# Kernel tuning notes

Measured on AMD Instinct MI355X. Metric: run time of the kernel, lower is better.

The kernel has to match this reference:

```python
import jax, jax.numpy as jnp
import numpy as np

N, R, E, DIN, DOUT, B = 40000, 16, 50000, 256, 256, 4


def setup_inputs() -> dict:
    key = jax.random.key(0)
    ks = jax.random.split(key, 7)
    xav = (2.0 / (DIN + DOUT)) ** 0.5  # xavier-ish scale
    x = jax.random.normal(ks[0], (N, DIN), jnp.float32)
    bases = jax.random.normal(ks[1], (B, DIN, DOUT), jnp.float32) * xav
    coeff = jax.random.normal(ks[2], (R, B), jnp.float32) * 0.5
    loop_weight = jax.random.normal(ks[3], (DIN, DOUT), jnp.float32) * xav
    h_bias = jnp.zeros((DOUT,), jnp.float32)
    edge_src = jax.random.randint(ks[4], (R, E), 0, N, dtype=jnp.int64)
    edge_dst = jax.random.randint(ks[5], (R, E), 0, N, dtype=jnp.int64)
    return {"x": x, "bases": bases, "coeff": coeff, "loop_weight": loop_weight,
            "h_bias": h_bias, "edge_src": edge_src, "edge_dst": edge_dst}


def reference(x, bases, coeff, loop_weight, h_bias, edge_src, edge_dst):
    # Basis decomposition: per-relation weight W_r = sum_b coeff[r,b] * bases[b]
    W = jnp.einsum('rb,bio->rio', coeff, bases)  # [R, DIN, DOUT]
    n = x.shape[0]

    def body(acc, rel):
        W_r, src, dst = rel
        # transform all nodes once, gather at edge sources
        m = (x @ W_r)[src]                                   # [E, DOUT]
        agg = jax.ops.segment_sum(m, dst, num_segments=n)    # [N, DOUT]
        deg = jax.ops.segment_sum(jnp.ones(src.shape, jnp.float32), dst,
                                  num_segments=n)            # in-degree per rel
        # norm='right': divide by dst in-degree (clamped to 1)
        return acc + agg / jnp.clip(deg, 1.0)[:, None], None

    h0 = jnp.zeros((n, loop_weight.shape[1]), x.dtype)
    h, _ = jax.lax.scan(body, h0, (W, edge_src, edge_dst))   # sum over relations
    h = h + x @ loop_weight + h_bias                         # self-loop + bias
    return jax.nn.relu(h)
```

## Files before the change

kernel.cpp:

```cpp
#include <hip/hip_runtime.h>

#define NN   40000
#define RR   16
#define EE   50000
#define DD   256
#define NB   4
#define KTOT (NB*DD + DD)
#define BM   64
#define BN   128
#define BK   32
#define NITER (KTOT/BK)

#define SCAN_BLK  40
#define SCAN_ELEM 1024

typedef __bf16 bf16x8 __attribute__((ext_vector_type(8)));
typedef float  f32x4  __attribute__((ext_vector_type(4)));
typedef float  f32x2  __attribute__((ext_vector_type(2)));
typedef unsigned short ushort_t;

__device__ inline unsigned short f2bf(float f) {
    unsigned int b = __builtin_bit_cast(unsigned int, f);
    b += 0x7FFFu + ((b >> 16) & 1u);
    return (unsigned short)(b >> 16);
}


#define CAST_BLKS ((NN * DD / 4 + DD * KTOT + 255) / 256)
#define DEG_BLKS  ((RR * EE + 255) / 256)

__global__ __launch_bounds__(256) void k_prep(const float* __restrict__ x,
                                              const float* __restrict__ bases,
                                              const float* __restrict__ lw,
                                              const int* __restrict__ edst,
                                              ushort_t* __restrict__ xb,
                                              ushort_t* __restrict__ Bt,
                                              int* __restrict__ deg) {
    int b = blockIdx.x;
    if (b < CAST_BLKS) {
        int t = b * 256 + threadIdx.x;
        const int NX = NN * DD / 4;
        if (t < NX) {
            float4 f = *(const float4*)(x + (size_t)t * 4);
            ushort4 o;
            o.x = f2bf(f.x); o.y = f2bf(f.y); o.z = f2bf(f.z); o.w = f2bf(f.w);
            *(ushort4*)(xb + (size_t)t * 4) = o;
        } else {
            int u = t - NX;
            if (u < DD * KTOT) {
                int o = u / KTOT, k = u - o * KTOT;
                float f = (k < NB * DD) ? bases[(size_t)k * DD + o]
                                        : lw[(size_t)(k - NB * DD) * DD + o];
                Bt[u] = f2bf(f);
            }
        }
    } else {
        int e = (b - CAST_BLKS) * 256 + threadIdx.x;
        if (e < RR * EE) {
            int r = e / EE;
            atomicAdd(&deg[r * NN + edst[e]], 1);
        }
    }
}

__global__ __launch_bounds__(256) void k_scanA(const int* __restrict__ deg,
                                               int* __restrict__ offsets,
                                               int* __restrict__ bsum) {
    __shared__ int part[256];
    int t = threadIdx.x, b = blockIdx.x;
    int g = b * SCAN_ELEM + t * 4;
    int4 h = {0, 0, 0, 0};
    if (g < NN) {
#pragma unroll
        for (int r = 0; r < RR; r++) {
            int4 d = *(const int4*)(deg + (size_t)r * NN + g);
            h.x += d.x; h.y += d.y; h.z += d.z; h.w += d.w;
        }
    }
    int s = h.x + h.y + h.z + h.w;
    part[t] = s;
    __syncthreads();
    for (int off = 1; off < 256; off <<= 1) {
        int v = (t >= off) ? part[t - off] : 0;
        __syncthreads();
        part[t] += v;
        __syncthreads();
    }
    int ex = part[t] - s;
    if (g < NN) {
        int4 o;
        o.x = ex;
        o.y = ex + h.x;
        o.z = ex + h.x + h.y;
        o.w = ex + h.x + h.y + h.z;
        *(int4*)(offsets + g) = o;
    }
    if (t == 255) bsum[b] = part[255];
}

__global__ __launch_bounds__(256) void k_scanB(const int* __restrict__ bsum,
                                               int* __restrict__ offsets,
                                               int* __restrict__ cursor) {
    __shared__ int sbase, stot;
    int t = threadIdx.x, b = blockIdx.x;
    if (t == 0) {
        int acc = 0, base = 0;
        for (int i = 0; i < SCAN_BLK; i++) {
            if (i == b) base = acc;
            acc += bsum[i];
        }
        sbase = base;
        stot = acc;
    }
    __syncthreads();
    int base = sbase;
    int g = b * SCAN_ELEM + t * 4;
    if (g < NN) {
        int4 o = *(const int4*)(offsets + g);
        o.x += base; o.y += base; o.z += base; o.w += base;
        *(int4*)(offsets + g) = o;
        *(int4*)(cursor + g) = o;
    }
    if (b == SCAN_BLK - 1 && t == 0) offsets[NN] = stot;
}

__global__ __launch_bounds__(256) void k_escatter(const int* __restrict__ esrc,
                                                  const int* __restrict__ edst,
                                                  int* __restrict__ cursor,
                                                  unsigned int* __restrict__ recs) {
    int e = blockIdx.x * blockDim.x + threadIdx.x;
    if (e >= RR * EE) return;
    int r = e / EE;
    int d = edst[e];
    int pos = atomicAdd(&cursor[d], 1);
    recs[pos] = (unsigned int)esrc[e] | ((unsigned int)r << 16);
}

__global__ __launch_bounds__(256) void k_gather(const ushort_t* __restrict__ xb,
                                                const float* __restrict__ coeff,
                                                const int* __restrict__ deg,
                                                const int* __restrict__ offsets,
                                                const unsigned int* __restrict__ recs,
                                                ushort_t* __restrict__ vb) {
    __shared__ float wtab[4][64];
    int lane = threadIdx.x & 63;
    int wv   = threadIdx.x >> 6;
    int n    = __builtin_amdgcn_readfirstlane(blockIdx.x * 4 + wv);

    {
        int r  = lane >> 2;
        int dg = deg[r * NN + n];
        float inv = 1.0f / (float)(dg > 0 ? dg : 1);
        wtab[wv][lane] = coeff[lane] * inv;
    }

    int beg = offsets[n], end = offsets[n + 1];
    f32x2 a[4][2];
#pragma unroll
    for (int b = 0; b < 4; b++) { a[b][0] = (f32x2){0,0}; a[b][1] = (f32x2){0,0}; }

    const float* wrow = &wtab[wv][0];
    const ushort_t* xl = xb + lane * 4;

    auto acc_edge = [&](uint2 u, float4 w) {
        f32x2 lo, hi;
        lo.x = __builtin_bit_cast(float, u.x << 16);
        lo.y = __builtin_bit_cast(float, u.x & 0xFFFF0000u);
        hi.x = __builtin_bit_cast(float, u.y << 16);
        hi.y = __builtin_bit_cast(float, u.y & 0xFFFF0000u);
        a[0][0] = lo * (f32x2){w.x, w.x} + a[0][0];
        a[0][1] = hi * (f32x2){w.x, w.x} + a[0][1];
        a[1][0] = lo * (f32x2){w.y, w.y} + a[1][0];
        a[1][1] = hi * (f32x2){w.y, w.y} + a[1][1];
        a[2][0] = lo * (f32x2){w.z, w.z} + a[2][0];
        a[2][1] = hi * (f32x2){w.z, w.z} + a[2][1];
        a[3][0] = lo * (f32x2){w.w, w.w} + a[3][0];
        a[3][1] = hi * (f32x2){w.w, w.w} + a[3][1];
    };

    int ei = beg;
    for (; ei + 4 <= end; ei += 4) {
        unsigned int r0 = recs[ei + 0];
        unsigned int r1 = recs[ei + 1];
        unsigned int r2 = recs[ei + 2];
        unsigned int r3 = recs[ei + 3];
        uint2 u0 = *(const uint2*)(xl + (size_t)(r0 & 0xFFFFu) * DD);
        uint2 u1 = *(const uint2*)(xl + (size_t)(r1 & 0xFFFFu) * DD);
        uint2 u2 = *(const uint2*)(xl + (size_t)(r2 & 0xFFFFu) * DD);
        uint2 u3 = *(const uint2*)(xl + (size_t)(r3 & 0xFFFFu) * DD);
        float4 w0 = *(const float4*)&wrow[(r0 >> 16) * 4];
        float4 w1 = *(const float4*)&wrow[(r1 >> 16) * 4];
        float4 w2 = *(const float4*)&wrow[(r2 >> 16) * 4];
        float4 w3 = *(const float4*)&wrow[(r3 >> 16) * 4];
        acc_edge(u0, w0);
        acc_edge(u1, w1);
        acc_edge(u2, w2);
        acc_edge(u3, w3);
    }
    for (; ei < end; ei++) {
        unsigned int r0 = recs[ei];
        uint2 u0 = *(const uint2*)(xl + (size_t)(r0 & 0xFFFFu) * DD);
        float4 w0 = *(const float4*)&wrow[(r0 >> 16) * 4];
        acc_edge(u0, w0);
    }

    ushort_t* vr = vb + (size_t)n * (NB * DD) + lane * 4;
#pragma unroll
    for (int b = 0; b < 4; b++) {
        ushort4 o;
        o.x = f2bf(a[b][0].x); o.y = f2bf(a[b][0].y);
        o.z = f2bf(a[b][1].x); o.w = f2bf(a[b][1].y);
        *(ushort4*)(vr + b * DD) = o;
    }
}

__global__ __launch_bounds__(256) void k_gemm(const ushort_t* __restrict__ vb,
                                              const ushort_t* __restrict__ xb,
                                              const ushort_t* __restrict__ Bt,
                                              const float* __restrict__ bias,
                                              float* __restrict__ out) {
    __shared__ ushort_t As[2][BM * BK];
    __shared__ ushort_t Bs[2][BN * BK];
    int tid  = threadIdx.x;
    int lane = tid & 63;
    int w    = tid >> 6;
    int wr   = w >> 1, wc = w & 1;
    int rowbase = blockIdx.x * BM;
    int nbase   = blockIdx.y * BN;
    int ml = lane & 15, q = lane >> 4;

    f32x4 acc[2][4];
#pragma unroll
    for (int i = 0; i < 2; i++)
#pragma unroll
        for (int j = 0; j < 4; j++) acc[i][j] = (f32x4){0,0,0,0};

    int srow = tid >> 2, sc = tid & 3;
    const ushort_t* bp0 = Bt + (size_t)(nbase + srow) * KTOT + sc * 8;
    const ushort_t* bp1 = Bt + (size_t)(nbase + 64 + srow) * KTOT + sc * 8;

    auto aptr = [&](int kb) {
        return (kb < NB * DD)
            ? vb + (size_t)(rowbase + srow) * (NB * DD) + kb + sc * 8
            : xb + (size_t)(rowbase + srow) * DD + (kb - NB * DD) + sc * 8;
    };

    int soff = srow * BK + ((sc ^ ((srow >> 2) & 3)) * 8);

    int aoff[2], boff[4];
#pragma unroll
    for (int i = 0; i < 2; i++) {
        int m = wr * 32 + i * 16 + ml;
        aoff[i] = m * BK + ((q ^ ((m >> 2) & 3)) * 8);
    }
#pragma unroll
    for (int j = 0; j < 4; j++) {
        int n = wc * 64 + j * 16 + ml;
        boff[j] = n * BK + ((q ^ ((n >> 2) & 3)) * 8);
    }

    uint4 a_e  = *(const uint4*)aptr(0);
    uint4 b0_e = *(const uint4*)(bp0);
    uint4 b1_e = *(const uint4*)(bp1);
    uint4 a_o  = *(const uint4*)aptr(BK);
    uint4 b0_o = *(const uint4*)(bp0 + BK);
    uint4 b1_o = *(const uint4*)(bp1 + BK);

    for (int it = 0; it < NITER; it += 2) {
        *(uint4*)&As[0][soff]           = a_e;
        *(uint4*)&Bs[0][soff]           = b0_e;
        *(uint4*)&Bs[0][64 * BK + soff] = b1_e;
        {
            int kb2 = (it + 2) * BK;
            if (kb2 < KTOT) {
                a_e  = *(const uint4*)aptr(kb2);
                b0_e = *(const uint4*)(bp0 + kb2);
                b1_e = *(const uint4*)(bp1 + kb2);
            }
        }
        __syncthreads();
        {
            bf16x8 af[2], bf[4];
#pragma unroll
            for (int i = 0; i < 2; i++) af[i] = *(const bf16x8*)&As[0][aoff[i]];
#pragma unroll
            for (int j = 0; j < 4; j++) bf[j] = *(const bf16x8*)&Bs[0][boff[j]];
#pragma unroll
            for (int i = 0; i < 2; i++)
#pragma unroll
                for (int j = 0; j < 4; j++)
                    acc[i][j] = __builtin_amdgcn_mfma_f32_16x16x32_bf16(af[i], bf[j], acc[i][j], 0, 0, 0);
        }
        *(uint4*)&As[1][soff]           = a_o;
        *(uint4*)&Bs[1][soff]           = b0_o;
        *(uint4*)&Bs[1][64 * BK + soff] = b1_o;
        {
            int kb3 = (it + 3) * BK;
            if (kb3 < KTOT) {
                a_o  = *(const uint4*)aptr(kb3);
                b0_o = *(const uint4*)(bp0 + kb3);
                b1_o = *(const uint4*)(bp1 + kb3);
            }
        }
        __syncthreads();
        {
            bf16x8 af[2], bf[4];
#pragma unroll
            for (int i = 0; i < 2; i++) af[i] = *(const bf16x8*)&As[1][aoff[i]];
#pragma unroll
            for (int j = 0; j < 4; j++) bf[j] = *(const bf16x8*)&Bs[1][boff[j]];
#pragma unroll
            for (int i = 0; i < 2; i++)
#pragma unroll
                for (int j = 0; j < 4; j++)
                    acc[i][j] = __builtin_amdgcn_mfma_f32_16x16x32_bf16(af[i], bf[j], acc[i][j], 0, 0, 0);
        }
    }

#pragma unroll
    for (int i = 0; i < 2; i++) {
#pragma unroll
        for (int r = 0; r < 4; r++) {
            int ng = rowbase + wr * 32 + i * 16 + q * 4 + r;
#pragma unroll
            for (int j = 0; j < 4; j++) {
                int o = nbase + wc * 64 + j * 16 + ml;
                float vv = acc[i][j][r] + bias[o];
                out[(size_t)ng * DD + o] = fmaxf(vv, 0.0f);
            }
        }
    }
}

extern "C" void kernel_launch(void* const* d_in, const int* in_sizes, int n_in,
                              void* d_out, int out_size, void* d_ws, size_t ws_size,
                              hipStream_t stream) {
    const float* x     = (const float*)d_in[0];
    const float* bases = (const float*)d_in[1];
    const float* coeff = (const float*)d_in[2];
    const float* lw    = (const float*)d_in[3];
    const float* bias  = (const float*)d_in[4];
    const int*   esrc  = (const int*)d_in[5];
    const int*   edst  = (const int*)d_in[6];
    float* out = (float*)d_out;

    char* ws = (char*)d_ws;
    ushort_t*     vb      = (ushort_t*)(ws);
    ushort_t*     xb      = (ushort_t*)(ws + 81920000);
    ushort_t*     Bt      = (ushort_t*)(ws + 102400000);
    int*          deg     = (int*)(ws + 103055360);
    int*          offsets = (int*)(ws + 105775360);
    int*          cursor  = (int*)(ws + 105935376);
    unsigned int* recs    = (unsigned int*)(ws + 106095376);
    int*          bsum    = (int*)(ws + 109295376);

    hipMemsetAsync(deg, 0, (size_t)RR * NN * sizeof(int), stream);

    int ne = RR * EE;
    k_prep<<<CAST_BLKS + DEG_BLKS, 256, 0, stream>>>(x, bases, lw, edst, xb, Bt, deg);
    k_scanA<<<SCAN_BLK, 256, 0, stream>>>(deg, offsets, bsum);
    k_scanB<<<SCAN_BLK, 256, 0, stream>>>(bsum, offsets, cursor);
    k_escatter<<<(ne + 255) / 256, 256, 0, stream>>>(esrc, edst, cursor, recs);
    k_gather<<<NN / 4, 256, 0, stream>>>(xb, coeff, deg, offsets, recs, vb);
    dim3 ggrid(NN / BM, DD / BN);
    k_gemm<<<ggrid, 256, 0, stream>>>(vb, xb, Bt, bias, out);
}
```

Measured before the change: 304.4 us.

## Use direct global-to-LDS loads and 128-row tiles in the final GEMM

Rewrites the final GEMM mainloop so global tiles go straight into LDS through global_load_lds, skipping the register staging step. The M tile is doubled to 128 rows, giving each wave a 64x64 output block (4x4 MFMA accumulators). The grid is swapped so blocks that share the same rows are launched next to each other, and the tail rows are clamped and masked. Each K step now waits on vmcnt(0) and a barrier, so the prefetch may not overlap well, and register pressure goes up.

```diff
diff --git a/kernel.cpp b/kernel.cpp
--- a/kernel.cpp
+++ b/kernel.cpp
@@ -1,4 +1,5 @@
 #include <hip/hip_runtime.h>
+#include <stdint.h>
 
 #define NN   40000
 #define RR   16
@@ -6,7 +7,7 @@
 #define DD   256
 #define NB   4
 #define KTOT (NB*DD + DD)
-#define BM   64
+#define BM   128
 #define BN   128
 #define BK   32
 #define NITER (KTOT/BK)
@@ -23,6 +24,13 @@
     unsigned int b = __builtin_bit_cast(unsigned int, f);
     b += 0x7FFFu + ((b >> 16) & 1u);
     return (unsigned short)(b >> 16);
+}
+
+__device__ __forceinline__ void gll16(const void* g, void* l) {
+    __builtin_amdgcn_global_load_lds(
+        (__attribute__((address_space(1))) void*)(uintptr_t)g,
+        (__attribute__((address_space(3))) void*)(uint32_t)(uintptr_t)l,
+        16, 0, 0);
 }
 
 
@@ -219,38 +227,39 @@
                                               const ushort_t* __restrict__ Bt,
                                               const float* __restrict__ bias,
                                               float* __restrict__ out) {
-    __shared__ ushort_t As[2][BM * BK];
-    __shared__ ushort_t Bs[2][BN * BK];
+    __shared__ __align__(16) ushort_t As[2][BM * BK];
+    __shared__ __align__(16) ushort_t Bs[2][BN * BK];
     int tid  = threadIdx.x;
     int lane = tid & 63;
     int w    = tid >> 6;
     int wr   = w >> 1, wc = w & 1;
-    int rowbase = blockIdx.x * BM;
-    int nbase   = blockIdx.y * BN;
+    int rowbase = blockIdx.y * BM;
+    int nbase   = blockIdx.x * BN;
     int ml = lane & 15, q = lane >> 4;
 
-    f32x4 acc[2][4];
-#pragma unroll
-    for (int i = 0; i < 2; i++)
-#pragma unroll
-        for (int j = 0; j < 4; j++) acc[i][j] = (f32x4){0,0,0,0};
-
-    int srow = tid >> 2, sc = tid & 3;
-    const ushort_t* bp0 = Bt + (size_t)(nbase + srow) * KTOT + sc * 8;
-    const ushort_t* bp1 = Bt + (size_t)(nbase + 64 + srow) * KTOT + sc * 8;
-
-    auto aptr = [&](int kb) {
-        return (kb < NB * DD)
-            ? vb + (size_t)(rowbase + srow) * (NB * DD) + kb + sc * 8
-            : xb + (size_t)(rowbase + srow) * DD + (kb - NB * DD) + sc * 8;
-    };
-
-    int soff = srow * BK + ((sc ^ ((srow >> 2) & 3)) * 8);
-
-    int aoff[2], boff[4];
-#pragma unroll
-    for (int i = 0; i < 2; i++) {
-        int m = wr * 32 + i * 16 + ml;
+    int srow  = tid >> 2;
+    int g     = (tid & 3) ^ ((tid >> 4) & 3);
+    int wbase = __builtin_amdgcn_readfirstlane(w << 10);
+
+    int arow0 = rowbase + srow;       if (arow0 >= NN) arow0 = NN - 1;
+    int arow1 = rowbase + 64 + srow;  if (arow1 >= NN) arow1 = NN - 1;
+    const ushort_t* pvA0 = vb + (size_t)arow0 * (NB * DD) + g * 8;
+    const ushort_t* pvA1 = vb + (size_t)arow1 * (NB * DD) + g * 8;
+    const ushort_t* pxA0 = xb + (size_t)arow0 * DD + g * 8;
+    const ushort_t* pxA1 = xb + (size_t)arow1 * DD + g * 8;
+    const ushort_t* pB0  = Bt + (size_t)(nbase + srow) * KTOT + g * 8;
+    const ushort_t* pB1  = Bt + (size_t)(nbase + 64 + srow) * KTOT + g * 8;
+
+    f32x4 acc[4][4];
+#pragma unroll
+    for (int i = 0; i < 4; i++)
+#pragma unroll
+        for (int j = 0; j < 4; j++) acc[i][j] = (f32x4){0, 0, 0, 0};
+
+    int aoff[4], boff[4];
+#pragma unroll
+    for (int i = 0; i < 4; i++) {
+        int m = wr * 64 + i * 16 + ml;
         aoff[i] = m * BK + ((q ^ ((m >> 2) & 3)) * 8);
     }
 #pragma unroll
@@ -259,74 +268,50 @@
         boff[j] = n * BK + ((q ^ ((n >> 2) & 3)) * 8);
     }
 
-    uint4 a_e  = *(const uint4*)aptr(0);
-    uint4 b0_e = *(const uint4*)(bp0);
-    uint4 b1_e = *(const uint4*)(bp1);
-    uint4 a_o  = *(const uint4*)aptr(BK);
-    uint4 b0_o = *(const uint4*)(bp0 + BK);
-    uint4 b1_o = *(const uint4*)(bp1 + BK);
-
-    for (int it = 0; it < NITER; it += 2) {
-        *(uint4*)&As[0][soff]           = a_e;
-        *(uint4*)&Bs[0][soff]           = b0_e;
-        *(uint4*)&Bs[0][64 * BK + soff] = b1_e;
-        {
-            int kb2 = (it + 2) * BK;
-            if (kb2 < KTOT) {
-                a_e  = *(const uint4*)aptr(kb2);
-                b0_e = *(const uint4*)(bp0 + kb2);
-                b1_e = *(const uint4*)(bp1 + kb2);
-            }
-        }
+    auto stage = [&](int s, int kb) {
+        const ushort_t* a0 = (kb < NB * DD) ? pvA0 + kb : pxA0 + (kb - NB * DD);
+        const ushort_t* a1 = (kb < NB * DD) ? pvA1 + kb : pxA1 + (kb - NB * DD);
+        char* ab = (char*)&As[s][0] + wbase;
+        char* bb = (char*)&Bs[s][0] + wbase;
+        gll16(a0,       ab);
+        gll16(a1,       ab + 4096);
+        gll16(pB0 + kb, bb);
+        gll16(pB1 + kb, bb + 4096);
+    };
+
+    stage(0, 0);
+    asm volatile("s_waitcnt vmcnt(0)" ::: "memory");
+    __syncthreads();
+
+    for (int it = 0; it < NITER; ++it) {
+        int cur = it & 1;
+        if (it + 1 < NITER) stage(cur ^ 1, (it + 1) * BK);
+        bf16x8 af[4], bf[4];
+#pragma unroll
+        for (int i = 0; i < 4; i++) af[i] = *(const bf16x8*)&As[cur][aoff[i]];
+#pragma unroll
+        for (int j = 0; j < 4; j++) bf[j] = *(const bf16x8*)&Bs[cur][boff[j]];
+#pragma unroll
+        for (int i = 0; i < 4; i++)
+#pragma unroll
+            for (int j = 0; j < 4; j++)
+                acc[i][j] = __builtin_amdgcn_mfma_f32_16x16x32_bf16(af[i], bf[j], acc[i][j], 0, 0, 0);
+        asm volatile("s_waitcnt vmcnt(0)" ::: "memory");
         __syncthreads();
-        {
-            bf16x8 af[2], bf[4];
-#pragma unroll
-            for (int i = 0; i < 2; i++) af[i] = *(const bf16x8*)&As[0][aoff[i]];
-#pragma unroll
-            for (int j = 0; j < 4; j++) bf[j] = *(const bf16x8*)&Bs[0][boff[j]];
-#pragma unroll
-            for (int i = 0; i < 2; i++)
-#pragma unroll
-                for (int j = 0; j < 4; j++)
-                    acc[i][j] = __builtin_amdgcn_mfma_f32_16x16x32_bf16(af[i], bf[j], acc[i][j], 0, 0, 0);
-        }
-        *(uint4*)&As[1][soff]           = a_o;
-        *(uint4*)&Bs[1][soff]           = b0_o;
-        *(uint4*)&Bs[1][64 * BK + soff] = b1_o;
-        {
-            int kb3 = (it + 3) * BK;
-            if (kb3 < KTOT) {
-                a_o  = *(const uint4*)aptr(kb3);
-                b0_o = *(const uint4*)(bp0 + kb3);
-                b1_o = *(const uint4*)(bp1 + kb3);
-            }
-        }
-        __syncthreads();
-        {
-            bf16x8 af[2], bf[4];
-#pragma unroll
-            for (int i = 0; i < 2; i++) af[i] = *(const bf16x8*)&As[1][aoff[i]];
-#pragma unroll
-            for (int j = 0; j < 4; j++) bf[j] = *(const bf16x8*)&Bs[1][boff[j]];
-#pragma unroll
-            for (int i = 0; i < 2; i++)
-#pragma unroll
-                for (int j = 0; j < 4; j++)
-                    acc[i][j] = __builtin_amdgcn_mfma_f32_16x16x32_bf16(af[i], bf[j], acc[i][j], 0, 0, 0);
-        }
-    }
-
-#pragma unroll
-    for (int i = 0; i < 2; i++) {
+    }
+
+#pragma unroll
+    for (int i = 0; i < 4; i++) {
 #pragma unroll
         for (int r = 0; r < 4; r++) {
-            int ng = rowbase + wr * 32 + i * 16 + q * 4 + r;
-#pragma unroll
-            for (int j = 0; j < 4; j++) {
-                int o = nbase + wc * 64 + j * 16 + ml;
-                float vv = acc[i][j][r] + bias[o];
-                out[(size_t)ng * DD + o] = fmaxf(vv, 0.0f);
+            int ng = rowbase + wr * 64 + i * 16 + q * 4 + r;
+            if (ng < NN) {
+#pragma unroll
+                for (int j = 0; j < 4; j++) {
+                    int o = nbase + wc * 64 + j * 16 + ml;
+                    float vv = acc[i][j][r] + bias[o];
+                    out[(size_t)ng * DD + o] = fmaxf(vv, 0.0f);
+                }
             }
         }
     }
@@ -362,6 +347,6 @@
     k_scanB<<<SCAN_BLK, 256, 0, stream>>>(bsum, offsets, cursor);
     k_escatter<<<(ne + 255) / 256, 256, 0, stream>>>(esrc, edst, cursor, recs);
     k_gather<<<NN / 4, 256, 0, stream>>>(xb, coeff, deg, offsets, recs, vb);
-    dim3 ggrid(NN / BM, DD / BN);
+    dim3 ggrid(DD / BN, (NN + BM - 1) / BM);
     k_gemm<<<ggrid, 256, 0, stream>>>(vb, xb, Bt, bias, out);
 }
```

Result: faster. 288.2 us (-5.3%).
